# Kernel optimization log

Measured on AMD Instinct MI355X. Metric: run time of the kernel, lower is better.

Reference implementation:

```python
import jax, jax.numpy as jnp
import numpy as np

BS, NA, HW, C, HEADS = 16, 256, 1024, 512, 8
FEAT_RES = 32  # hw = feat_res**2


def setup_inputs() -> dict:
    key = jax.random.key(0)
    ks = jax.random.split(key, 16)

    def lin_w(k, din, dout):
        return (jax.random.normal(k, (din, dout), jnp.float32) / np.sqrt(din)).astype(jnp.float32)

    inp = {
        "tok_agent": jax.random.normal(ks[0], (BS, NA, C), jnp.float32),
        "enc_feat_supp": jax.random.normal(ks[1], (BS, HW, C), jnp.float32),
        "enc_feat_query": jax.random.normal(ks[2], (BS, HW, C), jnp.float32),
        # projection weights stored as [in, out]
        "W_qa": lin_w(ks[3], C, C), "b_qa": jnp.zeros((C,), jnp.float32),
        "W_ks": lin_w(ks[4], C, C), "b_ks": jnp.zeros((C,), jnp.float32),
        "W_ka": lin_w(ks[5], C, C), "b_ka": jnp.zeros((C,), jnp.float32),
        "W_vs": lin_w(ks[6], C, C), "b_vs": jnp.zeros((C,), jnp.float32),
        # FFN: c -> 3c -> c
        "W_f1": lin_w(ks[7], C, 3 * C), "b_f1": jnp.zeros((3 * C,), jnp.float32),
        "W_f2": lin_w(ks[8], 3 * C, C), "b_f2": jnp.zeros((C,), jnp.float32),
    }
    return inp


def reference(tok_agent, enc_feat_supp, enc_feat_query,
              W_qa, b_qa, W_ks, b_ks, W_ka, b_ka, W_vs, b_vs,
              W_f1, b_f1, W_f2, b_f2):
    bs, na, c = tok_agent.shape
    hw = enc_feat_supp.shape[1]
    feat_res = int(round(np.sqrt(hw)))
    d_k_sqrt = np.float32(np.sqrt(c // HEADS))

    qa = tok_agent @ W_qa + b_qa                 # [bs, na, c]
    ks_ = enc_feat_supp @ W_ks + b_ks            # [bs, hw, c]
    qq = enc_feat_query @ W_qa + b_qa            # NOTE: original reuses qa_linear
    ka = tok_agent @ W_ka + b_ka                 # [bs, na, c]
    vs = enc_feat_supp @ W_vs + b_vs             # [bs, hw, c]

    scores_as = jnp.einsum('bac,bhc->bah', qa, ks_) / d_k_sqrt   # [bs, na, hw]
    scores_qa = jnp.einsum('bhc,bac->bha', qq, ka) / d_k_sqrt    # [bs, hw, na]

    # align_mat[b,i,j] = (argmax_a scores_as[b,a,i] == argmax_a scores_qa[b,j,a])
    a_idx = jnp.argmax(scores_as, axis=1)        # [bs, hw]
    b_idx = jnp.argmax(scores_qa, axis=2)        # [bs, hw]
    align = jnp.where(a_idx[:, :, None] == b_idx[:, None, :],
                      jnp.float32(0.0), jnp.float32(-1e6))       # [bs, hw, hw]

    # scores_sa @ scores_aq: [bs,hw,na] @ [bs,na,hw]
    logits = jnp.einsum('bai,bja->bij', scores_as, scores_qa)    # [bs, hw, hw]
    scores_qs = jax.nn.softmax(logits + align, axis=-1)

    # scores_qs^T @ vs : out[b,j,c] = sum_i scores_qs[b,i,j] * vs[b,i,c]
    dec = jnp.einsum('bij,bic->bjc', scores_qs, vs)              # [bs, hw, c]
    dec = jax.nn.relu(dec @ W_f1 + b_f1) @ W_f2 + b_f2           # FFN (dropout = eval identity)

    # raw memory reinterpretation, as in torch .view
    return dec.reshape(bs, c, feat_res, -1)
```

## Files before the change

kernel.cpp:

```cpp
#include <hip/hip_runtime.h>

typedef float          f32x4  __attribute__((ext_vector_type(4)));
typedef short          bf16x8 __attribute__((ext_vector_type(8)));
typedef _Float16       f16x8  __attribute__((ext_vector_type(8)));
typedef unsigned short u16x4  __attribute__((ext_vector_type(4)));

static constexpr int kBS = 16;
static constexpr int kHW = 1024;

__device__ __forceinline__ unsigned short f2bf(float x) {
  union { float f; unsigned int u; } v; v.f = x;
  unsigned int r = v.u + 0x7fffu + ((v.u >> 16) & 1u);
  return (unsigned short)(r >> 16);
}
__device__ __forceinline__ float bf2f(unsigned short h) {
  union { unsigned int u; float f; } v; v.u = ((unsigned int)h) << 16;
  return v.f;
}
__device__ __forceinline__ unsigned short h2u(_Float16 h) {
  union { _Float16 h; unsigned short u; } v; v.h = h; return v.u;
}
__device__ __forceinline__ unsigned int fmono(float f) {
  union { float f; unsigned int u; } v; v.f = f;
  return (v.u & 0x80000000u) ? ~v.u : (v.u | 0x80000000u);
}

__device__ __forceinline__ void split2h(float x, unsigned short& u0, unsigned short& u1) {
  _Float16 h0 = (_Float16)x;
  if (fabsf(x) < 6.1035156e-05f) h0 = (_Float16)0.f;
  const float r = (x - (float)h0) * 4096.f;
  u0 = h2u(h0);
  u1 = h2u((_Float16)r);
}

__global__ __launch_bounds__(256)
void split_act2h(const f32x4* __restrict__ X, u16x4* __restrict__ P0,
                 u16x4* __restrict__ P1, int n4)
{
  int i = blockIdx.x * 256 + threadIdx.x;
  if (i >= n4) return;
  f32x4 x = X[i];
  u16x4 s0, s1;
#pragma unroll
  for (int u = 0; u < 4; ++u) {
    unsigned short a, b;
    split2h(x[u], a, b);
    s0[u] = a; s1[u] = b;
  }
  P0[i] = s0; P1[i] = s1;
}

__global__ __launch_bounds__(256)
void split_wT2h(const float* __restrict__ Wm, unsigned short* __restrict__ T0,
                unsigned short* __restrict__ T1, int K, int N)
{
  __shared__ float ts[32][33];
  const int k0 = blockIdx.x * 32, n0 = blockIdx.y * 32;
  const int tx = threadIdx.x, ty = threadIdx.y;
#pragma unroll
  for (int r = 0; r < 4; ++r)
    ts[ty + r * 8][tx] = Wm[(size_t)(k0 + ty + r * 8) * N + n0 + tx];
  __syncthreads();
#pragma unroll
  for (int r = 0; r < 4; ++r) {
    const int n = ty + r * 8;
    const size_t off = (size_t)(n0 + n) * K + k0 + tx;
    unsigned short a, b;
    split2h(ts[tx][n], a, b);
    T0[off] = a; T1[off] = b;
  }
}

template<bool F16>
__global__ __launch_bounds__(256)
void split_wT1(const float* __restrict__ Wm, unsigned short* __restrict__ T0,
               int K, int N)
{
  __shared__ float ts[32][33];
  const int k0 = blockIdx.x * 32, n0 = blockIdx.y * 32;
  const int tx = threadIdx.x, ty = threadIdx.y;
#pragma unroll
  for (int r = 0; r < 4; ++r)
    ts[ty + r * 8][tx] = Wm[(size_t)(k0 + ty + r * 8) * N + n0 + tx];
  __syncthreads();
#pragma unroll
  for (int r = 0; r < 4; ++r) {
    const int n = ty + r * 8;
    const float x = ts[tx][n];
    const size_t off = (size_t)(n0 + n) * K + k0 + tx;
    T0[off] = F16 ? h2u((_Float16)x) : f2bf(x);
  }
}

__device__ __forceinline__ void stage_tile(const unsigned short* src, int K,
                                           unsigned short* ldst, int wv, int lane)
{
#pragma unroll
  for (int i = 0; i < 2; ++i) {
    const int s   = wv * 128 + i * 64 + lane;
    const int row = s >> 2;
    const int gc  = ((s & 3) ^ ((row >> 1) & 3)) * 8;
    __builtin_amdgcn_global_load_lds(
        (const __attribute__((address_space(1))) void*)(src + (size_t)row * K + gc),
        (__attribute__((address_space(3))) void*)(ldst + ((wv * 128 + i * 64) << 3)),
        16, 0, 0);
  }
}

template<int ORD, int KU, int DEPTH, int OUTM, bool BIAS, bool RELU, bool F16IN>
__global__ __launch_bounds__(256)
void gke(const unsigned short* __restrict__ A0, const unsigned short* __restrict__ A1,
         const unsigned short* __restrict__ B0, const unsigned short* __restrict__ B1,
         const float* __restrict__ bias,
         float* __restrict__ Cf, unsigned short* __restrict__ O0,
         unsigned short* __restrict__ O1, unsigned long long* __restrict__ keys,
         int K, int ldc, long sA, long sB, long sC, long sBias, float scale)
{
  constexpr int NP   = ORD + 1;
  constexpr int NT   = 2 * NP;
  constexpr int TPP  = KU * NT;
  constexpr int LPP  = TPP * 2;
  static_assert(DEPTH == 2 || DEPTH == 4, "DEPTH in {2,4}");
  static_assert(LPP == 4 || LPP == 8 || LPP == 16, "vmcnt literals");
  extern __shared__ __align__(16) unsigned short lds[];

  const int tid  = threadIdx.x;
  const int wv   = tid >> 6, lane = tid & 63;
  const int wr   = wv >> 1,  wc   = wv & 1;
  const int cr   = lane & 15, cg  = lane >> 4;
  const int bm   = blockIdx.x * 128, bn = blockIdx.y * 128;

  const size_t zA = (size_t)blockIdx.z * (size_t)sA;
  const size_t zB = (size_t)blockIdx.z * (size_t)sB;
  const size_t zC = (size_t)blockIdx.z * (size_t)sC;
  const size_t zBias = (size_t)blockIdx.z * (size_t)sBias;

  const unsigned short* srcs[NT];
  srcs[0] = A0 + zA + (size_t)bm * K;
  if (NP == 2) srcs[1] = A1 + zA + (size_t)bm * K;
  srcs[NP + 0] = B0 + zB + (size_t)bn * K;
  if (NP == 2) srcs[NP + 1] = B1 + zB + (size_t)bn * K;

  f32x4 acc0[4][4], acc1[4][4];
#pragma unroll
  for (int i = 0; i < 4; ++i)
#pragma unroll
    for (int j = 0; j < 4; ++j)
#pragma unroll
      for (int r = 0; r < 4; ++r) {
        acc0[i][j][r] = 0.f;
        if (ORD == 1) acc1[i][j][r] = 0.f;
      }

#define STAGE_PH(ph, buf)                                                       \
  {                                                                             \
    _Pragma("unroll")                                                           \
    for (int u = 0; u < KU; ++u)                                                \
      _Pragma("unroll")                                                         \
      for (int t = 0; t < NT; ++t)                                              \
        stage_tile(srcs[t] + ((ph) * KU + u) * 32, K,                           \
                   lds + (size_t)((buf) * TPP + u * NT + t) * 4096, wv, lane);  \
  }
#define LOADA(u, pa)                                                            \
  {                                                                             \
    _Pragma("unroll")                                                           \
    for (int f = 0; f < 4; ++f) {                                               \
      const int ra = wr * 64 + f * 16 + cr;                                     \
      af[f] = *(const bf16x8*)&lb[(size_t)((u) * NT + (pa)) * 4096 +            \
                                  (ra * 4 + (cg ^ ((ra >> 1) & 3))) * 8];       \
    }                                                                           \
  }
#define DOPB(u, pb, ACC)                                                        \
  {                                                                             \
    bf16x8 bfr[4];                                                              \
    _Pragma("unroll")                                                           \
    for (int f = 0; f < 4; ++f) {                                               \
      const int rb = wc * 64 + f * 16 + cr;                                     \
      bfr[f] = *(const bf16x8*)&lb[(size_t)((u) * NT + NP + (pb)) * 4096 +      \
                                   (rb * 4 + (cg ^ ((rb >> 1) & 3))) * 8];      \
    }                                                                           \
    _Pragma("unroll")                                                           \
    for (int i = 0; i < 4; ++i)                                                 \
      _Pragma("unroll")                                                         \
      for (int j = 0; j < 4; ++j) {                                             \
        if constexpr (F16IN)                                                    \
          ACC[i][j] = __builtin_amdgcn_mfma_f32_16x16x32_f16(                   \
              __builtin_bit_cast(f16x8, af[i]), __builtin_bit_cast(f16x8, bfr[j]), \
              ACC[i][j], 0, 0, 0);                                              \
        else                                                                    \
          ACC[i][j] = __builtin_amdgcn_mfma_f32_16x16x32_bf16(af[i], bfr[j],    \
              ACC[i][j], 0, 0, 0);                                              \
      }                                                                         \
  }
#define COMPUTE_PH(buf)                                                         \
  {                                                                             \
    const unsigned short* lb = lds + (size_t)(buf) * TPP * 4096;                \
    bf16x8 af[4];                                                               \
    _Pragma("unroll")                                                           \
    for (int u = 0; u < KU; ++u) {                                              \
      if constexpr (ORD == 1) {                                                 \
        LOADA(u, 0); DOPB(u, 0, acc0); DOPB(u, 1, acc1);                        \
        LOADA(u, 1); DOPB(u, 0, acc1);                                          \
      } else {                                                                  \
        LOADA(u, 0); DOPB(u, 0, acc0);                                          \
      }                                                                         \
    }                                                                           \
  }

  const int nph = K / (32 * KU);
#pragma unroll
  for (int d = 0; d < DEPTH; ++d)
    if (d < nph) STAGE_PH(d, d);

  for (int ph = 0; ph < nph; ++ph) {
    const int rem = nph - 1 - ph;
    const int fut = rem < (DEPTH - 1) ? rem : (DEPTH - 1);
    if constexpr (LPP == 4) {
      if (fut >= 3)      asm volatile("s_waitcnt vmcnt(12)" ::: "memory");
      else if (fut == 2) asm volatile("s_waitcnt vmcnt(8)" ::: "memory");
      else if (fut == 1) asm volatile("s_waitcnt vmcnt(4)" ::: "memory");
      else               asm volatile("s_waitcnt vmcnt(0)" ::: "memory");
    } else if constexpr (LPP == 8) {
      if (fut >= 3)      asm volatile("s_waitcnt vmcnt(24)" ::: "memory");
      else if (fut == 2) asm volatile("s_waitcnt vmcnt(16)" ::: "memory");
      else if (fut == 1) asm volatile("s_waitcnt vmcnt(8)" ::: "memory");
      else               asm volatile("s_waitcnt vmcnt(0)" ::: "memory");
    } else {
      if (fut >= 1)      asm volatile("s_waitcnt vmcnt(16)" ::: "memory");
      else               asm volatile("s_waitcnt vmcnt(0)" ::: "memory");
    }
    __builtin_amdgcn_sched_barrier(0);
    __builtin_amdgcn_s_barrier();
    COMPUTE_PH(ph & (DEPTH - 1));
    __builtin_amdgcn_s_barrier();
    __builtin_amdgcn_sched_barrier(0);
    if (ph + DEPTH < nph) STAGE_PH(ph + DEPTH, ph & (DEPTH - 1));
  }
#undef STAGE_PH
#undef LOADA
#undef DOPB
#undef COMPUTE_PH

  const float RS = 2.44140625e-4f;
  float* CfB = Cf + zC;
  unsigned short* O0B = O0 + zC;
  unsigned short* O1B = O1 + zC;

  if constexpr (OUTM == 5) {
#pragma unroll
    for (int fm = 0; fm < 4; ++fm) {
      const int m0 = bm + wr * 64 + fm * 16 + 4 * cg;
      unsigned long long bk[4] = {0ull, 0ull, 0ull, 0ull};
#pragma unroll
      for (int fn = 0; fn < 4; ++fn) {
        const int n = bn + wc * 64 + fn * 16 + cr;
#pragma unroll
        for (int r = 0; r < 4; ++r) {
          const float x = (acc0[fm][fn][r] + acc1[fm][fn][r] * RS) * scale;
          unsigned short a, b;
          split2h(x, a, b);
          const size_t off = (size_t)(m0 + r) * ldc + n;
          O0B[off] = a; O1B[off] = b;
          const unsigned long long k =
              ((unsigned long long)fmono(x) << 32) | (unsigned)(255 - n);
          if (k > bk[r]) bk[r] = k;
        }
      }
#pragma unroll
      for (int r = 0; r < 4; ++r) {
        unsigned long long k = bk[r];
#pragma unroll
        for (int o = 1; o < 16; o <<= 1) {
          const unsigned long long ok =
              (unsigned long long)__shfl_xor((long long)k, o, 16);
          if (ok > k) k = ok;
        }
        if ((lane & 15) == 0)
          atomicMax(keys + (size_t)blockIdx.z * 1024 + (m0 + r), k);
      }
    }
    return;
  }

#pragma unroll
  for (int fm = 0; fm < 4; ++fm) {
#pragma unroll
    for (int fn = 0; fn < 4; ++fn) {
      const int n  = bn + wc * 64 + fn * 16 + cr;
      const int m0 = bm + wr * 64 + fm * 16 + 4 * cg;
      float bv = 0.f;
      if (BIAS) bv = bias[zBias + n];
      if (OUTM == 4) {
        u16x4 o;
#pragma unroll
        for (int r = 0; r < 4; ++r) {
          float x = acc0[fm][fn][r];
          if constexpr (ORD == 1) x += acc1[fm][fn][r] * RS;
          x = x * scale + bv;
          if (RELU) x = fmaxf(x, 0.f);
          o[r] = f2bf(x);
        }
        *(u16x4*)(O0B + (size_t)n * ldc + m0) = o;
      } else {
#pragma unroll
        for (int r = 0; r < 4; ++r) {
          float x = acc0[fm][fn][r];
          if constexpr (ORD == 1) x += acc1[fm][fn][r] * RS;
          x = x * scale + bv;
          if (RELU) x = fmaxf(x, 0.f);
          const size_t off = (size_t)(m0 + r) * ldc + n;
          if (OUTM == 0) CfB[off] = x;
          else if (OUTM == 3) O0B[off] = f2bf(x);
          else {
            unsigned short a, b;
            split2h(x, a, b);
            O0B[off] = a; O1B[off] = b;
            if (OUTM == 2) CfB[off] = x;
          }
        }
      }
    }
  }
}

__global__ __launch_bounds__(256)
void softmax_T(const float* __restrict__ Lg, const unsigned long long* __restrict__ keysA,
               const unsigned long long* __restrict__ keysB,
               unsigned short* __restrict__ PT, int ihalf)
{
  __shared__ int bj[1024];
  __shared__ unsigned short tile[1024 * 17];
  const int tid = threadIdx.x;
  const int i0  = blockIdx.x * 16;
  const int b   = blockIdx.y;
  const int r   = tid >> 4;
  const int l16 = tid & 15;

  for (int j = tid; j < 1024; j += 256)
    bj[j] = 255 - (int)(keysB[(b << 10) + j] & 0xFFFFFFFFull);
  __syncthreads();

  const int ai = 255 - (int)(keysA[(b << 10) + (ihalf << 9) + i0 + r] & 0xFFFFFFFFull);
  const float* Lr = Lg + ((size_t)b * 512 + i0 + r) * 1024;
  const int jb = l16 * 64;

  float x[64];
  float mx = -3.0e38f;
#pragma unroll
  for (int q = 0; q < 16; ++q) {
    f32x4 f = *(const f32x4*)(Lr + jb + (q << 2));
#pragma unroll
    for (int u = 0; u < 4; ++u) {
      const int j = jb + (q << 2) + u;
      float t = f[u];
      if (bj[j] != ai) t -= 1e6f;
      x[(q << 2) + u] = t;
      mx = fmaxf(mx, t);
    }
  }
#pragma unroll
  for (int off = 8; off >= 1; off >>= 1) mx = fmaxf(mx, __shfl_xor(mx, off));
  float s = 0.f;
#pragma unroll
  for (int k = 0; k < 64; ++k) { float e = expf(x[k] - mx); x[k] = e; s += e; }
#pragma unroll
  for (int off = 8; off >= 1; off >>= 1) s += __shfl_xor(s, off);
  const float inv = 1.f / s;

#pragma unroll
  for (int k = 0; k < 64; ++k)
    tile[(jb + k) * 17 + r] = f2bf(x[k] * inv);
  __syncthreads();

  for (int j = tid; j < 1024; j += 256) {
    const unsigned short* tp = &tile[j * 17];
    unsigned int w[8];
#pragma unroll
    for (int q = 0; q < 8; ++q)
      w[q] = (unsigned int)tp[2 * q] | ((unsigned int)tp[2 * q + 1] << 16);
    const size_t off = ((size_t)b << 20) + ((size_t)j << 10) + (ihalf << 9) + i0;
    unsigned int* dst = (unsigned int*)(PT + off);
    *(uint4*)dst       = make_uint4(w[0], w[1], w[2], w[3]);
    *((uint4*)dst + 1) = make_uint4(w[4], w[5], w[6], w[7]);
  }
}

extern "C" void kernel_launch(void* const* d_in, const int* in_sizes, int n_in,
                              void* d_out, int out_size, void* d_ws, size_t ws_size,
                              hipStream_t stream)
{
  (void)in_sizes; (void)n_in; (void)out_size; (void)ws_size;

  const float* tok  = (const float*)d_in[0];
  const float* supp = (const float*)d_in[1];
  const float* qry  = (const float*)d_in[2];
  const float* W_qa = (const float*)d_in[3];
  const float* b_qa = (const float*)d_in[4];
  const float* W_ks = (const float*)d_in[5];
  const float* b_ks = (const float*)d_in[6];
  const float* W_ka = (const float*)d_in[7];
  const float* b_ka = (const float*)d_in[8];
  const float* W_vs = (const float*)d_in[9];
  const float* b_vs = (const float*)d_in[10];
  const float* W_f1 = (const float*)d_in[11];
  const float* b_f1 = (const float*)d_in[12];
  const float* W_f2 = (const float*)d_in[13];
  const float* b_f2 = (const float*)d_in[14];

  auto kProj  = &gke<1,1,2,1,true ,false,true >;
  auto kScore = &gke<1,2,2,5,false,false,true >;
  auto kLogit = &gke<1,1,2,0,false,false,true >;
  auto kVsT   = &gke<0,1,2,4,true ,false,true >;
  auto kPV    = &gke<0,1,2,3,false,false,false>;
  auto kFFN1  = &gke<0,1,2,3,true ,true ,false>;
  auto kFFN2  = &gke<0,1,2,0,true ,false,false>;
  hipFuncSetAttribute((const void*)kProj,  hipFuncAttributeMaxDynamicSharedMemorySize, 65536);
  hipFuncSetAttribute((const void*)kScore, hipFuncAttributeMaxDynamicSharedMemorySize, 131072);
  hipFuncSetAttribute((const void*)kLogit, hipFuncAttributeMaxDynamicSharedMemorySize, 65536);
  hipFuncSetAttribute((const void*)kVsT,   hipFuncAttributeMaxDynamicSharedMemorySize, 32768);
  hipFuncSetAttribute((const void*)kPV,    hipFuncAttributeMaxDynamicSharedMemorySize, 32768);
  hipFuncSetAttribute((const void*)kFFN1,  hipFuncAttributeMaxDynamicSharedMemorySize, 32768);
  hipFuncSetAttribute((const void*)kFFN2,  hipFuncAttributeMaxDynamicSharedMemorySize, 32768);

  char* W = (char*)d_ws;
  constexpr size_t MiB = 1048576;
  auto U = [&](double off) { return (unsigned short*)(W + (size_t)(off * MiB)); };
  auto F = [&](double off) { return (float*)(W + (size_t)(off * MiB)); };
  auto KY = [&](double off) { return (unsigned long long*)(W + (size_t)(off * MiB)); };

  const double oTOK0=0, oTOK1=4, oSUP0=0, oPT=0;
  const double oWQAT=16, oWKAT=17.5, oWKST=19, oWVST=20.5;
  const double oQA0=22, oQA1=26, oDEC=32, oKA0=34, oKA1=38;
  const double oQRY0=46, oQRY1=62, oQTP0=46, oQTP1=54;
  const double oSUP1=62, oVST=62, oSAP0=78, oSAP1=86;
  const double oQQ0=94, oQQ1=110, oLG=94, oMID=62;
  const double oWF1=142, oWF2=143.5, oBIA=148, oKEYB=148.5, oKEYA=148.75;
  const double hP = 0.5;

  const dim3 B256(256), BW(32, 8);
  float* dummyF = F(oLG);
  unsigned short* dummyU = U(oLG);
  unsigned long long* dummyK = KY(oLG);

  hipMemcpyAsync(W + (size_t)(oBIA * MiB), b_qa, 2048, hipMemcpyDeviceToDevice, stream);
  hipMemcpyAsync(W + (size_t)(oBIA * MiB) + 2048, b_ka, 2048, hipMemcpyDeviceToDevice, stream);
  hipMemsetAsync(KY(oKEYB), 0, kBS * kHW * 8, stream);
  hipMemsetAsync(KY(oKEYA), 0, kBS * kHW * 8, stream);

  split_wT2h<<<dim3(16,16), BW, 0, stream>>>(W_qa, U(oWQAT), U(oWQAT+hP), 512, 512);
  split_wT2h<<<dim3(16,16), BW, 0, stream>>>(W_ka, U(oWKAT), U(oWKAT+hP), 512, 512);
  split_wT2h<<<dim3(16,16), BW, 0, stream>>>(W_ks, U(oWKST), U(oWKST+hP), 512, 512);
  split_wT1<true><<<dim3(16,16), BW, 0, stream>>>(W_vs, U(oWVST), 512, 512);
  split_act2h<<<dim3(2048), B256, 0, stream>>>((const f32x4*)tok, (u16x4*)U(oTOK0), (u16x4*)U(oTOK1), 524288);
  kProj<<<dim3(32,4,2), B256, 65536, stream>>>(
      U(oTOK0),U(oTOK1), U(oWQAT),U(oWQAT+hP),
      F(oBIA), dummyF, U(oQA0),U(oQA1), dummyK, 512, 512, 0, 786432, 6291456, 512, 1.f);
  split_act2h<<<dim3(8192), B256, 0, stream>>>((const f32x4*)qry, (u16x4*)U(oQRY0), (u16x4*)U(oQRY1), 2097152);
  kProj<<<dim3(128,4,1), B256, 65536, stream>>>(
      U(oQRY0),U(oQRY1), U(oWQAT),U(oWQAT+hP),
      b_qa, dummyF, U(oQQ0),U(oQQ1), dummyK, 512, 512, 0,0,0,0, 1.f);
  kScore<<<dim3(8,2,16), B256, 131072, stream>>>(
      U(oQQ0),U(oQQ1), U(oKA0),U(oKA1),
      nullptr, dummyF, U(oQTP0),U(oQTP1), KY(oKEYB), 512, 256,
      524288, 131072, 262144, 0, 0.125f);
  split_act2h<<<dim3(8192), B256, 0, stream>>>((const f32x4*)supp, (u16x4*)U(oSUP0), (u16x4*)U(oSUP1), 2097152);
  kProj<<<dim3(128,4,1), B256, 65536, stream>>>(
      U(oSUP0),U(oSUP1), U(oWKST),U(oWKST+hP),
      b_ks, dummyF, U(oQQ0),U(oQQ1), dummyK, 512, 512, 0,0,0,0, 1.f);
  kVsT<<<dim3(8,4,16), B256, 32768, stream>>>(
      U(oSUP0),dummyU, U(oWVST),dummyU,
      b_vs, dummyF, U(oVST),dummyU, dummyK, 512, 1024,
      524288, 0, 524288, 0, 1.f);
  kScore<<<dim3(8,2,16), B256, 131072, stream>>>(
      U(oQQ0),U(oQQ1), U(oQA0),U(oQA1),
      nullptr, dummyF, U(oSAP0),U(oSAP1), KY(oKEYA), 512, 256,
      524288, 131072, 262144, 0, 0.125f);
  split_wT1<false><<<dim3(16,48), BW, 0, stream>>>(W_f1, U(oWF1), 512, 1536);
  split_wT1<false><<<dim3(48,16), BW, 0, stream>>>(W_f2, U(oWF2), 1536, 512);
  for (int h = 0; h < 2; ++h) {
    kLogit<<<dim3(4,8,16), B256, 65536, stream>>>(
        U(oSAP0) + (size_t)h*512*256, U(oSAP1) + (size_t)h*512*256,
        U(oQTP0), U(oQTP1),
        nullptr, F(oLG), dummyU,dummyU, dummyK, 256, 1024,
        262144, 262144, 524288, 0, 1.f);
    softmax_T<<<dim3(32,16), B256, 0, stream>>>(F(oLG), KY(oKEYA), KY(oKEYB), U(oPT), h);
  }
  kPV<<<dim3(8,4,16), B256, 32768, stream>>>(
      U(oPT),dummyU, U(oVST),dummyU,
      nullptr, dummyF, U(oDEC),dummyU, dummyK, 1024, 512,
      1048576, 524288, 524288, 0, 1.f);
  kFFN1<<<dim3(128,12,1), B256, 32768, stream>>>(
      U(oDEC),dummyU, U(oWF1),dummyU,
      b_f1, dummyF, U(oMID),dummyU, dummyK, 512, 1536, 0,0,0,0, 1.f);
  kFFN2<<<dim3(128,4,1), B256, 32768, stream>>>(
      U(oMID),dummyU, U(oWF2),dummyU,
      b_f2, (float*)d_out, dummyU,dummyU, dummyK, 1536, 512, 0,0,0,0, 1.f);
}
```

Measured before the change: 407.1 us.

## Add triple-buffered single-precision GEMM kernel for VsT, PV and FFN stages

Adds a dedicated gkp GEMM kernel for the single-order (ORD=0) matmuls. It uses a three-slot LDS ring with register double-buffered fragments, so global-to-LDS loads for tile t+3 overlap MFMA work on the current tile. The VsT, PV and FFN1/FFN2 launches now use it with 48KB of dynamic LDS instead of the generic gke template. The gke epilogue is trimmed to the paths still in use. The extra LDS may reduce occupancy, and the hand-counted vmcnt waits have to stay correct for every K.

After: 409.3 us. About the same (+0.5%).

```diff
diff --git a/kernel.cpp b/kernel.cpp
--- a/kernel.cpp
+++ b/kernel.cpp
@@ -104,6 +104,134 @@
         (const __attribute__((address_space(1))) void*)(src + (size_t)row * K + gc),
         (__attribute__((address_space(3))) void*)(ldst + ((wv * 128 + i * 64) << 3)),
         16, 0, 0);
+  }
+}
+
+template<int OUTM, bool BIAS, bool RELU, bool F16IN>
+__global__ __launch_bounds__(256)
+void gkp(const unsigned short* __restrict__ A0, const unsigned short* __restrict__ B0,
+         const float* __restrict__ bias,
+         float* __restrict__ Cf, unsigned short* __restrict__ O0,
+         int K, int ldc, long sA, long sB, long sC, float scale)
+{
+  extern __shared__ __align__(16) unsigned short lds[];
+
+  const int tid  = threadIdx.x;
+  const int wv   = tid >> 6, lane = tid & 63;
+  const int wr   = wv >> 1,  wc   = wv & 1;
+  const int cr   = lane & 15, cg  = lane >> 4;
+  const int bm   = blockIdx.x * 128, bn = blockIdx.y * 128;
+
+  const unsigned short* Ap = A0 + (size_t)blockIdx.z * (size_t)sA + (size_t)bm * K;
+  const unsigned short* Bp = B0 + (size_t)blockIdx.z * (size_t)sB + (size_t)bn * K;
+  const size_t zC = (size_t)blockIdx.z * (size_t)sC;
+
+  f32x4 acc[4][4];
+#pragma unroll
+  for (int i = 0; i < 4; ++i)
+#pragma unroll
+    for (int j = 0; j < 4; ++j)
+#pragma unroll
+      for (int r = 0; r < 4; ++r) acc[i][j][r] = 0.f;
+
+  bf16x8 fX[8], fY[8];
+
+#define STAGE_SLOT(t, sl)                                                      \
+  {                                                                            \
+    stage_tile(Ap + (t) * 32, K, lds + (size_t)(sl) * 8192,        wv, lane);  \
+    stage_tile(Bp + (t) * 32, K, lds + (size_t)(sl) * 8192 + 4096, wv, lane);  \
+  }
+#define READF(FR, sl)                                                          \
+  {                                                                            \
+    const unsigned short* lb = lds + (size_t)(sl) * 8192;                      \
+    _Pragma("unroll")                                                          \
+    for (int f = 0; f < 4; ++f) {                                              \
+      const int ra = wr * 64 + f * 16 + cr;                                    \
+      FR[f] = *(const bf16x8*)&lb[(ra * 4 + (cg ^ ((ra >> 1) & 3))) * 8];      \
+      const int rb = wc * 64 + f * 16 + cr;                                    \
+      FR[4 + f] = *(const bf16x8*)&lb[4096 + (rb * 4 + (cg ^ ((rb >> 1) & 3))) * 8]; \
+    }                                                                          \
+  }
+#define DOMM(FR)                                                               \
+  {                                                                            \
+    _Pragma("unroll")                                                          \
+    for (int i = 0; i < 4; ++i)                                                \
+      _Pragma("unroll")                                                        \
+      for (int j = 0; j < 4; ++j) {                                            \
+        if constexpr (F16IN)                                                   \
+          acc[i][j] = __builtin_amdgcn_mfma_f32_16x16x32_f16(                  \
+              __builtin_bit_cast(f16x8, FR[i]), __builtin_bit_cast(f16x8, FR[4 + j]), \
+              acc[i][j], 0, 0, 0);                                             \
+        else                                                                   \
+          acc[i][j] = __builtin_amdgcn_mfma_f32_16x16x32_bf16(FR[i], FR[4 + j], \
+              acc[i][j], 0, 0, 0);                                             \
+      }                                                                        \
+  }
+
+  const int nt = K >> 5;
+  STAGE_SLOT(0, 0);
+  STAGE_SLOT(1, 1);
+  STAGE_SLOT(2, 2);
+  asm volatile("s_waitcnt vmcnt(8)" ::: "memory");
+  __builtin_amdgcn_sched_barrier(0);
+  __builtin_amdgcn_s_barrier();
+  READF(fX, 0);
+
+  for (int t = 0; t < nt; t += 2) {
+    if (t + 2 < nt) asm volatile("s_waitcnt vmcnt(4)" ::: "memory");
+    else            asm volatile("s_waitcnt vmcnt(0)" ::: "memory");
+    __builtin_amdgcn_sched_barrier(0);
+    __builtin_amdgcn_s_barrier();
+    READF(fY, (t + 1) % 3);
+    DOMM(fX);
+    __builtin_amdgcn_s_barrier();
+    __builtin_amdgcn_sched_barrier(0);
+    if (t + 3 < nt) STAGE_SLOT(t + 3, t % 3);
+    if (t + 3 < nt) asm volatile("s_waitcnt vmcnt(4)" ::: "memory");
+    else            asm volatile("s_waitcnt vmcnt(0)" ::: "memory");
+    __builtin_amdgcn_sched_barrier(0);
+    __builtin_amdgcn_s_barrier();
+    if (t + 2 < nt) READF(fX, (t + 2) % 3);
+    DOMM(fY);
+    __builtin_amdgcn_s_barrier();
+    __builtin_amdgcn_sched_barrier(0);
+    if (t + 4 < nt) STAGE_SLOT(t + 4, (t + 1) % 3);
+  }
+#undef STAGE_SLOT
+#undef READF
+#undef DOMM
+
+  float* CfB = Cf + zC;
+  unsigned short* O0B = O0 + zC;
+#pragma unroll
+  for (int fm = 0; fm < 4; ++fm) {
+#pragma unroll
+    for (int fn = 0; fn < 4; ++fn) {
+      const int n  = bn + wc * 64 + fn * 16 + cr;
+      const int m0 = bm + wr * 64 + fm * 16 + 4 * cg;
+      float bv = 0.f;
+      if (BIAS) bv = bias[n];
+      f32x4 v = acc[fm][fn];
+      if (OUTM == 4) {
+        u16x4 o;
+#pragma unroll
+        for (int r = 0; r < 4; ++r) {
+          float x = v[r] * scale + bv;
+          if (RELU) x = fmaxf(x, 0.f);
+          o[r] = f2bf(x);
+        }
+        *(u16x4*)(O0B + (size_t)n * ldc + m0) = o;
+      } else {
+#pragma unroll
+        for (int r = 0; r < 4; ++r) {
+          float x = v[r] * scale + bv;
+          if (RELU) x = fmaxf(x, 0.f);
+          const size_t off = (size_t)(m0 + r) * ldc + n;
+          if (OUTM == 0) CfB[off] = x;
+          else O0B[off] = f2bf(x);
+        }
+      }
+    }
   }
 }
 
@@ -290,33 +418,18 @@
       const int m0 = bm + wr * 64 + fm * 16 + 4 * cg;
       float bv = 0.f;
       if (BIAS) bv = bias[zBias + n];
-      if (OUTM == 4) {
-        u16x4 o;
-#pragma unroll
-        for (int r = 0; r < 4; ++r) {
-          float x = acc0[fm][fn][r];
-          if constexpr (ORD == 1) x += acc1[fm][fn][r] * RS;
-          x = x * scale + bv;
-          if (RELU) x = fmaxf(x, 0.f);
-          o[r] = f2bf(x);
-        }
-        *(u16x4*)(O0B + (size_t)n * ldc + m0) = o;
-      } else {
-#pragma unroll
-        for (int r = 0; r < 4; ++r) {
-          float x = acc0[fm][fn][r];
-          if constexpr (ORD == 1) x += acc1[fm][fn][r] * RS;
-          x = x * scale + bv;
-          if (RELU) x = fmaxf(x, 0.f);
-          const size_t off = (size_t)(m0 + r) * ldc + n;
-          if (OUTM == 0) CfB[off] = x;
-          else if (OUTM == 3) O0B[off] = f2bf(x);
-          else {
-            unsigned short a, b;
-            split2h(x, a, b);
-            O0B[off] = a; O1B[off] = b;
-            if (OUTM == 2) CfB[off] = x;
-          }
+#pragma unroll
+      for (int r = 0; r < 4; ++r) {
+        float x = acc0[fm][fn][r];
+        if constexpr (ORD == 1) x += acc1[fm][fn][r] * RS;
+        x = x * scale + bv;
+        if (RELU) x = fmaxf(x, 0.f);
+        const size_t off = (size_t)(m0 + r) * ldc + n;
+        if (OUTM == 0) CfB[off] = x;
+        else {
+          unsigned short a, b;
+          split2h(x, a, b);
+          O0B[off] = a; O1B[off] = b;
         }
       }
     }
@@ -410,17 +523,17 @@
   auto kProj  = &gke<1,1,2,1,true ,false,true >;
   auto kScore = &gke<1,2,2,5,false,false,true >;
   auto kLogit = &gke<1,1,2,0,false,false,true >;
-  auto kVsT   = &gke<0,1,2,4,true ,false,true >;
-  auto kPV    = &gke<0,1,2,3,false,false,false>;
-  auto kFFN1  = &gke<0,1,2,3,true ,true ,false>;
-  auto kFFN2  = &gke<0,1,2,0,true ,false,false>;
+  auto kVsT   = &gkp<4,true ,false,true >;
+  auto kPV    = &gkp<3,false,false,false>;
+  auto kFFN1  = &gkp<3,true ,true ,false>;
+  auto kFFN2  = &gkp<0,true ,false,false>;
   hipFuncSetAttribute((const void*)kProj,  hipFuncAttributeMaxDynamicSharedMemorySize, 65536);
   hipFuncSetAttribute((const void*)kScore, hipFuncAttributeMaxDynamicSharedMemorySize, 131072);
   hipFuncSetAttribute((const void*)kLogit, hipFuncAttributeMaxDynamicSharedMemorySize, 65536);
-  hipFuncSetAttribute((const void*)kVsT,   hipFuncAttributeMaxDynamicSharedMemorySize, 32768);
-  hipFuncSetAttribute((const void*)kPV,    hipFuncAttributeMaxDynamicSharedMemorySize, 32768);
-  hipFuncSetAttribute((const void*)kFFN1,  hipFuncAttributeMaxDynamicSharedMemorySize, 32768);
-  hipFuncSetAttribute((const void*)kFFN2,  hipFuncAttributeMaxDynamicSharedMemorySize, 32768);
+  hipFuncSetAttribute((const void*)kVsT,   hipFuncAttributeMaxDynamicSharedMemorySize, 49152);
+  hipFuncSetAttribute((const void*)kPV,    hipFuncAttributeMaxDynamicSharedMemorySize, 49152);
+  hipFuncSetAttribute((const void*)kFFN1,  hipFuncAttributeMaxDynamicSharedMemorySize, 49152);
+  hipFuncSetAttribute((const void*)kFFN2,  hipFuncAttributeMaxDynamicSharedMemorySize, 49152);
 
   char* W = (char*)d_ws;
   constexpr size_t MiB = 1048576;
@@ -467,10 +580,9 @@
   kProj<<<dim3(128,4,1), B256, 65536, stream>>>(
       U(oSUP0),U(oSUP1), U(oWKST),U(oWKST+hP),
       b_ks, dummyF, U(oQQ0),U(oQQ1), dummyK, 512, 512, 0,0,0,0, 1.f);
-  kVsT<<<dim3(8,4,16), B256, 32768, stream>>>(
-      U(oSUP0),dummyU, U(oWVST),dummyU,
-      b_vs, dummyF, U(oVST),dummyU, dummyK, 512, 1024,
-      524288, 0, 524288, 0, 1.f);
+  kVsT<<<dim3(8,4,16), B256, 49152, stream>>>(
+      U(oSUP0), U(oWVST), b_vs, dummyF, U(oVST), 512, 1024,
+      524288, 0, 524288, 1.f);
   kScore<<<dim3(8,2,16), B256, 131072, stream>>>(
       U(oQQ0),U(oQQ1), U(oQA0),U(oQA1),
       nullptr, dummyF, U(oSAP0),U(oSAP1), KY(oKEYA), 512, 256,
@@ -485,14 +597,11 @@
         262144, 262144, 524288, 0, 1.f);
     softmax_T<<<dim3(32,16), B256, 0, stream>>>(F(oLG), KY(oKEYA), KY(oKEYB), U(oPT), h);
   }
-  kPV<<<dim3(8,4,16), B256, 32768, stream>>>(
-      U(oPT),dummyU, U(oVST),dummyU,
-      nullptr, dummyF, U(oDEC),dummyU, dummyK, 1024, 512,
-      1048576, 524288, 524288, 0, 1.f);
-  kFFN1<<<dim3(128,12,1), B256, 32768, stream>>>(
-      U(oDEC),dummyU, U(oWF1),dummyU,
-      b_f1, dummyF, U(oMID),dummyU, dummyK, 512, 1536, 0,0,0,0, 1.f);
-  kFFN2<<<dim3(128,4,1), B256, 32768, stream>>>(
-      U(oMID),dummyU, U(oWF2),dummyU,
-      b_f2, (float*)d_out, dummyU,dummyU, dummyK, 1536, 512, 0,0,0,0, 1.f);
-}
+  kPV<<<dim3(8,4,16), B256, 49152, stream>>>(
+      U(oPT), U(oVST), nullptr, dummyF, U(oDEC), 1024, 512,
+      1048576, 524288, 524288, 1.f);
+  kFFN1<<<dim3(128,12,1), B256, 49152, stream>>>(
+      U(oDEC), U(oWF1), b_f1, dummyF, U(oMID), 512, 1536, 0,0,0, 1.f);
+  kFFN2<<<dim3(128,4,1), B256, 49152, stream>>>(
+      U(oMID), U(oWF2), b_f2, (float*)d_out, dummyU, 1536, 512, 0,0,0, 1.f);
+}
```

## Batch score GEMMs into one launch and process logits in a single pass

Applied to the files above, without the earlier changes.

Reorders the workspace so the two score GEMMs (query-vs-agent and support-vs-agent) run as one launch over a doubled batch dimension. The logit GEMM and the transposed softmax now cover all 1024 rows in one launch each instead of two half passes, which needs a larger fp32 logit buffer. It also drops a redundant fp32 store in the split-output epilogue. The aim is fewer kernel launches and larger grids for better occupancy, at the cost of more workspace memory and intricate buffer aliasing.

Measured after the change: 396.0 us. 1.03x faster.

```diff
diff --git a/kernel.cpp b/kernel.cpp
--- a/kernel.cpp
+++ b/kernel.cpp
@@ -315,7 +315,6 @@
             unsigned short a, b;
             split2h(x, a, b);
             O0B[off] = a; O1B[off] = b;
-            if (OUTM == 2) CfB[off] = x;
           }
         }
       }
@@ -326,7 +325,7 @@
 __global__ __launch_bounds__(256)
 void softmax_T(const float* __restrict__ Lg, const unsigned long long* __restrict__ keysA,
                const unsigned long long* __restrict__ keysB,
-               unsigned short* __restrict__ PT, int ihalf)
+               unsigned short* __restrict__ PT)
 {
   __shared__ int bj[1024];
   __shared__ unsigned short tile[1024 * 17];
@@ -340,8 +339,8 @@
     bj[j] = 255 - (int)(keysB[(b << 10) + j] & 0xFFFFFFFFull);
   __syncthreads();
 
-  const int ai = 255 - (int)(keysA[(b << 10) + (ihalf << 9) + i0 + r] & 0xFFFFFFFFull);
-  const float* Lr = Lg + ((size_t)b * 512 + i0 + r) * 1024;
+  const int ai = 255 - (int)(keysA[(b << 10) + i0 + r] & 0xFFFFFFFFull);
+  const float* Lr = Lg + ((size_t)(b << 10) + i0 + r) * 1024;
   const int jb = l16 * 64;
 
   float x[64];
@@ -378,7 +377,7 @@
 #pragma unroll
     for (int q = 0; q < 8; ++q)
       w[q] = (unsigned int)tp[2 * q] | ((unsigned int)tp[2 * q + 1] << 16);
-    const size_t off = ((size_t)b << 20) + ((size_t)j << 10) + (ihalf << 9) + i0;
+    const size_t off = ((size_t)b << 20) + ((size_t)j << 10) + i0;
     unsigned int* dst = (unsigned int*)(PT + off);
     *(uint4*)dst       = make_uint4(w[0], w[1], w[2], w[3]);
     *((uint4*)dst + 1) = make_uint4(w[4], w[5], w[6], w[7]);
@@ -428,71 +427,54 @@
   auto F = [&](double off) { return (float*)(W + (size_t)(off * MiB)); };
   auto KY = [&](double off) { return (unsigned long long*)(W + (size_t)(off * MiB)); };
 
-  const double oTOK0=0, oTOK1=4, oSUP0=0, oPT=0;
-  const double oWQAT=16, oWKAT=17.5, oWKST=19, oWVST=20.5;
-  const double oQA0=22, oQA1=26, oDEC=32, oKA0=34, oKA1=38;
-  const double oQRY0=46, oQRY1=62, oQTP0=46, oQTP1=54;
-  const double oSUP1=62, oVST=62, oSAP0=78, oSAP1=86;
-  const double oQQ0=94, oQQ1=110, oLG=94, oMID=62;
-  const double oWF1=142, oWF2=143.5, oBIA=148, oKEYB=148.5, oKEYA=148.75;
-  const double hP = 0.5;
-
   const dim3 B256(256), BW(32, 8);
-  float* dummyF = F(oLG);
-  unsigned short* dummyU = U(oLG);
-  unsigned long long* dummyK = KY(oLG);
-
-  hipMemcpyAsync(W + (size_t)(oBIA * MiB), b_qa, 2048, hipMemcpyDeviceToDevice, stream);
-  hipMemcpyAsync(W + (size_t)(oBIA * MiB) + 2048, b_ka, 2048, hipMemcpyDeviceToDevice, stream);
-  hipMemsetAsync(KY(oKEYB), 0, kBS * kHW * 8, stream);
-  hipMemsetAsync(KY(oKEYA), 0, kBS * kHW * 8, stream);
-
-  split_wT2h<<<dim3(16,16), BW, 0, stream>>>(W_qa, U(oWQAT), U(oWQAT+hP), 512, 512);
-  split_wT2h<<<dim3(16,16), BW, 0, stream>>>(W_ka, U(oWKAT), U(oWKAT+hP), 512, 512);
-  split_wT2h<<<dim3(16,16), BW, 0, stream>>>(W_ks, U(oWKST), U(oWKST+hP), 512, 512);
-  split_wT1<true><<<dim3(16,16), BW, 0, stream>>>(W_vs, U(oWVST), 512, 512);
-  split_act2h<<<dim3(2048), B256, 0, stream>>>((const f32x4*)tok, (u16x4*)U(oTOK0), (u16x4*)U(oTOK1), 524288);
+  float* dummyF = F(78);
+  unsigned short* dummyU = U(78);
+  unsigned long long* dummyK = KY(78);
+
+  hipMemcpyAsync(W + (size_t)(148.0 * MiB), b_ka, 2048, hipMemcpyDeviceToDevice, stream);
+  hipMemcpyAsync(W + (size_t)(148.0 * MiB) + 2048, b_qa, 2048, hipMemcpyDeviceToDevice, stream);
+  hipMemsetAsync(KY(148.5), 0, 32 * 1024 * 8, stream);
+
+  split_wT2h<<<dim3(16,16), BW, 0, stream>>>(W_ka, U(16),   U(17),   512, 512);
+  split_wT2h<<<dim3(16,16), BW, 0, stream>>>(W_qa, U(16.5), U(17.5), 512, 512);
+  split_wT2h<<<dim3(16,16), BW, 0, stream>>>(W_ks, U(18),   U(18.5), 512, 512);
+  split_wT1<true><<<dim3(16,16), BW, 0, stream>>>(W_vs, U(19), 512, 512);
+  split_act2h<<<dim3(2048), B256, 0, stream>>>((const f32x4*)tok, (u16x4*)U(0), (u16x4*)U(4), 524288);
   kProj<<<dim3(32,4,2), B256, 65536, stream>>>(
-      U(oTOK0),U(oTOK1), U(oWQAT),U(oWQAT+hP),
-      F(oBIA), dummyF, U(oQA0),U(oQA1), dummyK, 512, 512, 0, 786432, 6291456, 512, 1.f);
-  split_act2h<<<dim3(8192), B256, 0, stream>>>((const f32x4*)qry, (u16x4*)U(oQRY0), (u16x4*)U(oQRY1), 2097152);
+      U(0),U(4), U(16),U(17),
+      F(148), dummyF, U(22),U(30), dummyK, 512, 512, 0, 262144, 2097152, 512, 1.f);
+  split_act2h<<<dim3(8192), B256, 0, stream>>>((const f32x4*)qry, (u16x4*)U(46), (u16x4*)U(62), 2097152);
   kProj<<<dim3(128,4,1), B256, 65536, stream>>>(
-      U(oQRY0),U(oQRY1), U(oWQAT),U(oWQAT+hP),
-      b_qa, dummyF, U(oQQ0),U(oQQ1), dummyK, 512, 512, 0,0,0,0, 1.f);
-  kScore<<<dim3(8,2,16), B256, 131072, stream>>>(
-      U(oQQ0),U(oQQ1), U(oKA0),U(oKA1),
-      nullptr, dummyF, U(oQTP0),U(oQTP1), KY(oKEYB), 512, 256,
+      U(46),U(62), U(16.5),U(17.5),
+      b_qa, dummyF, U(78),U(110), dummyK, 512, 512, 0,0,0,0, 1.f);
+  split_act2h<<<dim3(8192), B256, 0, stream>>>((const f32x4*)supp, (u16x4*)U(0), (u16x4*)U(46), 2097152);
+  kProj<<<dim3(128,4,1), B256, 65536, stream>>>(
+      U(0),U(46), U(18),U(18.5),
+      b_ks, dummyF, U(94),U(126), dummyK, 512, 512, 0,0,0,0, 1.f);
+  kVsT<<<dim3(8,4,16), B256, 32768, stream>>>(
+      U(0),dummyU, U(19),dummyU,
+      b_vs, dummyF, U(62),dummyU, dummyK, 512, 1024,
+      524288, 0, 524288, 0, 1.f);
+  kScore<<<dim3(8,2,32), B256, 131072, stream>>>(
+      U(78),U(110), U(22),U(30),
+      nullptr, dummyF, U(0),U(46), KY(148.5), 512, 256,
       524288, 131072, 262144, 0, 0.125f);
-  split_act2h<<<dim3(8192), B256, 0, stream>>>((const f32x4*)supp, (u16x4*)U(oSUP0), (u16x4*)U(oSUP1), 2097152);
-  kProj<<<dim3(128,4,1), B256, 65536, stream>>>(
-      U(oSUP0),U(oSUP1), U(oWKST),U(oWKST+hP),
-      b_ks, dummyF, U(oQQ0),U(oQQ1), dummyK, 512, 512, 0,0,0,0, 1.f);
-  kVsT<<<dim3(8,4,16), B256, 32768, stream>>>(
-      U(oSUP0),dummyU, U(oWVST),dummyU,
-      b_vs, dummyF, U(oVST),dummyU, dummyK, 512, 1024,
-      524288, 0, 524288, 0, 1.f);
-  kScore<<<dim3(8,2,16), B256, 131072, stream>>>(
-      U(oQQ0),U(oQQ1), U(oQA0),U(oQA1),
-      nullptr, dummyF, U(oSAP0),U(oSAP1), KY(oKEYA), 512, 256,
-      524288, 131072, 262144, 0, 0.125f);
-  split_wT1<false><<<dim3(16,48), BW, 0, stream>>>(W_f1, U(oWF1), 512, 1536);
-  split_wT1<false><<<dim3(48,16), BW, 0, stream>>>(W_f2, U(oWF2), 1536, 512);
-  for (int h = 0; h < 2; ++h) {
-    kLogit<<<dim3(4,8,16), B256, 65536, stream>>>(
-        U(oSAP0) + (size_t)h*512*256, U(oSAP1) + (size_t)h*512*256,
-        U(oQTP0), U(oQTP1),
-        nullptr, F(oLG), dummyU,dummyU, dummyK, 256, 1024,
-        262144, 262144, 524288, 0, 1.f);
-    softmax_T<<<dim3(32,16), B256, 0, stream>>>(F(oLG), KY(oKEYA), KY(oKEYB), U(oPT), h);
-  }
+  split_wT1<false><<<dim3(16,48), BW, 0, stream>>>(W_f1, U(142), 512, 1536);
+  split_wT1<false><<<dim3(48,16), BW, 0, stream>>>(W_f2, U(143.5), 1536, 512);
+  kLogit<<<dim3(8,8,16), B256, 65536, stream>>>(
+      U(8),U(54), U(0),U(46),
+      nullptr, F(78), dummyU,dummyU, dummyK, 256, 1024,
+      262144, 262144, 1048576, 0, 1.f);
+  softmax_T<<<dim3(64,16), B256, 0, stream>>>(F(78), KY(148.5) + 16384, KY(148.5), U(0));
   kPV<<<dim3(8,4,16), B256, 32768, stream>>>(
-      U(oPT),dummyU, U(oVST),dummyU,
-      nullptr, dummyF, U(oDEC),dummyU, dummyK, 1024, 512,
+      U(0),dummyU, U(62),dummyU,
+      nullptr, dummyF, U(32),dummyU, dummyK, 1024, 512,
       1048576, 524288, 524288, 0, 1.f);
   kFFN1<<<dim3(128,12,1), B256, 32768, stream>>>(
-      U(oDEC),dummyU, U(oWF1),dummyU,
-      b_f1, dummyF, U(oMID),dummyU, dummyK, 512, 1536, 0,0,0,0, 1.f);
+      U(32),dummyU, U(142),dummyU,
+      b_f1, dummyF, U(94),dummyU, dummyK, 512, 1536, 0,0,0,0, 1.f);
   kFFN2<<<dim3(128,4,1), B256, 32768, stream>>>(
-      U(oMID),dummyU, U(oWF2),dummyU,
+      U(94),dummyU, U(143.5),dummyU,
       b_f2, (float*)d_out, dummyU,dummyU, dummyK, 1536, 512, 0,0,0,0, 1.f);
 }
```
